# Kernel tuning notes

Measured on AMD Instinct MI355X. Metric: run time of the kernel, lower is better.

Reference implementation:

```python
import jax, jax.numpy as jnp
import numpy as np

N_EMBD = 2048
N_HEAD = 16
N_KV_HEAD = 4
HEAD_DIM = N_EMBD // N_HEAD  # 128
BLOCK_SIZE = 2048
B, T = 4, 2048


def _rope_cache(max_pos, head_dim):
    inv_freq = 1.0 / (10000.0 ** (np.arange(0, head_dim, 2, dtype=np.float32) / head_dim))
    t = np.arange(max_pos, dtype=np.float32)
    freqs = np.repeat(np.outer(t, inv_freq), 2, axis=-1)  # [max_pos, head_dim], interleaved repeat
    return jnp.asarray(np.cos(freqs)), jnp.asarray(np.sin(freqs))

COS, SIN = _rope_cache(BLOCK_SIZE, HEAD_DIM)


def _apply_rope(x, pos):
    # x: [B, nh, T, hd]; matches torch module: cos/sin repeat-interleaved, rotate by halves
    Tq = x.shape[2]
    cos = jax.lax.dynamic_slice_in_dim(COS, pos, Tq, axis=0)[None, None]  # [1,1,T,hd]
    sin = jax.lax.dynamic_slice_in_dim(SIN, pos, Tq, axis=0)[None, None]
    hd = x.shape[-1]
    x1, x2 = x[..., : hd // 2], x[..., hd // 2 :]
    return x * cos + jnp.concatenate([-x2, x1], axis=-1) * sin


def setup_inputs() -> dict:
    key = jax.random.key(0)
    ks = jax.random.split(key, 5)
    scale = 1.0 / np.sqrt(N_EMBD)
    return {
        "x": jax.random.normal(ks[0], (B, T, N_EMBD), dtype=jnp.float32),
        "Wq": jax.random.normal(ks[1], (N_EMBD, N_EMBD), dtype=jnp.float32) * scale,
        "Wk": jax.random.normal(ks[2], (N_EMBD, N_KV_HEAD * HEAD_DIM), dtype=jnp.float32) * scale,
        "Wv": jax.random.normal(ks[3], (N_EMBD, N_KV_HEAD * HEAD_DIM), dtype=jnp.float32) * scale,
        "Wo": jax.random.normal(ks[4], (N_EMBD, N_EMBD), dtype=jnp.float32) * scale,
        "pos": 0,
    }


def reference(x, Wq, Wk, Wv, Wo, pos):
    Bx, Tx, C = x.shape
    q = (x @ Wq).reshape(Bx, Tx, N_HEAD, HEAD_DIM).transpose(0, 2, 1, 3)      # [B,nh,T,hd]
    k = (x @ Wk).reshape(Bx, Tx, N_KV_HEAD, HEAD_DIM).transpose(0, 2, 1, 3)   # [B,nkv,T,hd]
    v = (x @ Wv).reshape(Bx, Tx, N_KV_HEAD, HEAD_DIM).transpose(0, 2, 1, 3)
    q = _apply_rope(q, pos)
    k = _apply_rope(k, pos)
    # GQA: expand kv heads to query heads (cache=None -> causal prefill)
    rep = N_HEAD // N_KV_HEAD
    kr = jnp.repeat(k, rep, axis=1)
    vr = jnp.repeat(v, rep, axis=1)
    scores = jnp.einsum("bhqd,bhkd->bhqk", q, kr) / np.sqrt(HEAD_DIM)
    causal = jnp.tril(jnp.ones((Tx, Tx), dtype=bool))
    scores = jnp.where(causal[None, None], scores, jnp.finfo(scores.dtype).min)
    att = jax.nn.softmax(scores, axis=-1)
    out = jnp.einsum("bhqk,bhkd->bhqd", att, vr)          # [B,nh,T,hd]
    y = out.transpose(0, 2, 1, 3).reshape(Bx, Tx, C)
    return y @ Wo
```

## Files before the change

kernel.cpp:

```cpp
#include <hip/hip_runtime.h>
#include <math.h>

#define TT 2048

typedef __attribute__((ext_vector_type(8))) short bfrag;
typedef __attribute__((ext_vector_type(4))) float facc;

#define NEG_BIG (-1.0e30f)

typedef __attribute__((address_space(1))) const void gas_void;
typedef __attribute__((address_space(3))) void las_void;

__device__ __forceinline__ void gl_lds16(const void* g, void* l) {
    __builtin_amdgcn_global_load_lds((gas_void*)g, (las_void*)l, 16, 0, 0);
}

__device__ __forceinline__ unsigned short f2b(float f) {
    union { float f; unsigned int i; } v; v.f = f;
    unsigned int b = v.i;
    return (unsigned short)((b + 0x7FFFu + ((b >> 16) & 1u)) >> 16);
}
__device__ __forceinline__ void cvt8_f32(const float* __restrict__ p, unsigned short* d) {
    float4 lo = *(const float4*)p, hi = *(const float4*)(p + 4);
    d[0] = f2b(lo.x); d[1] = f2b(lo.y); d[2] = f2b(lo.z); d[3] = f2b(lo.w);
    d[4] = f2b(hi.x); d[5] = f2b(hi.y); d[6] = f2b(hi.z); d[7] = f2b(hi.w);
}

__global__ __launch_bounds__(256) void k_cvt(const float* __restrict__ in,
                                             unsigned short* __restrict__ out, int n8) {
    int c = blockIdx.x * 256 + threadIdx.x;
    if (c < n8) {
        unsigned short t[8];
        cvt8_f32(in + (size_t)c * 8, t);
        *(uint4*)(out + (size_t)c * 8) = *(const uint4*)t;
    }
}

__global__ __launch_bounds__(256) void k_wt(const float* __restrict__ W,
                                            unsigned short* __restrict__ WT, int N) {
    __shared__ alignas(16) unsigned short tile[64][72];
    int r0 = blockIdx.y * 64, c0 = blockIdx.x * 64;
    int tid = threadIdx.x;
    for (int i = 0; i < 2; ++i) {
        int c = tid + i * 256;
        int row = c >> 3, c8 = (c & 7) * 8;
        unsigned short t[8];
        cvt8_f32(W + (size_t)(r0 + row) * N + c0 + c8, t);
        *(uint4*)&tile[row][c8] = *(const uint4*)t;
    }
    __syncthreads();
    for (int i = 0; i < 2; ++i) {
        int c = tid + i * 256;
        int col = c >> 3, r8 = (c & 7) * 8;
        unsigned short t[8];
        for (int j = 0; j < 8; ++j) t[j] = tile[r8 + j][col];
        *(uint4*)(WT + (size_t)(c0 + col) * 2048 + r0 + r8) = *(const uint4*)t;
    }
}

__global__ __launch_bounds__(256) void k_vt(const unsigned short* __restrict__ QKV,
                                            unsigned short* __restrict__ VbT) {
    __shared__ alignas(16) unsigned short tile[64][72];
    int r0 = blockIdx.y * 64, c0 = blockIdx.x * 64;
    int tid = threadIdx.x;
    for (int i = 0; i < 2; ++i) {
        int c = tid + i * 256;
        int row = c >> 3, c8 = (c & 7) * 8;
        *(uint4*)&tile[row][c8] =
            *(const uint4*)(QKV + (size_t)(r0 + row) * 3072 + 2560 + c0 + c8);
    }
    __syncthreads();
    for (int i = 0; i < 2; ++i) {
        int c = tid + i * 256;
        int col = c >> 3, r8 = (c & 7) * 8;
        unsigned short t[8];
        for (int j = 0; j < 8; ++j) t[j] = tile[r8 + j][col];
        *(uint4*)(VbT + (size_t)(c0 + col) * 8192 + r0 + r8) = *(const uint4*)t;
    }
}

__global__ __launch_bounds__(256) void k_gemm2ph(const unsigned short* __restrict__ A,
                                                 const unsigned short* __restrict__ Bt,
                                                 void* __restrict__ Cmat,
                                                 int M, int N, int K, int outF) {
    __shared__ union SM {
        struct { unsigned short A[2][128][64]; unsigned short B[2][128][64]; } s;
        unsigned short ct[32][136];
        float          ctf[32][136];
    } sm;
    int tid = threadIdx.x;
    int w = tid >> 6, lane = tid & 63, quad = lane >> 4, l15 = lane & 15;
    int m0 = blockIdx.y * 128, n0 = blockIdx.x * 128;
    int wm = (w >> 1) * 64, wn = (w & 1) * 64;

    int srow   = lane >> 3;
    int schunk = (lane & 7) ^ (lane >> 3);

    facc acc[4][4];
#pragma unroll
    for (int mi = 0; mi < 4; ++mi)
#pragma unroll
        for (int ni = 0; ni < 4; ++ni)
#pragma unroll
            for (int r = 0; r < 4; ++r) acc[mi][ni][r] = 0.f;

    auto stage = [&](int bb, int k0) {
#pragma unroll
        for (int i = 0; i < 4; ++i) {
            int row = w * 32 + i * 8;
            gl_lds16(A  + (size_t)(m0 + row + srow) * K + k0 + schunk * 8, &sm.s.A[bb][row][0]);
            gl_lds16(Bt + (size_t)(n0 + row + srow) * K + k0 + schunk * 8, &sm.s.B[bb][row][0]);
        }
    };

    int NT = K >> 6;
    stage(0, 0);
    __syncthreads();

    for (int t = 0; t < NT; ++t) {
        int cur = t & 1;
        if (t + 1 < NT) stage(cur ^ 1, (t + 1) * 64);

        bfrag af[4][2], bf[4][2];
#pragma unroll
        for (int mi = 0; mi < 4; ++mi)
#pragma unroll
            for (int kc = 0; kc < 2; ++kc)
                af[mi][kc] = *(const bfrag*)&sm.s.A[cur][wm + mi * 16 + l15][((kc * 4 + quad) ^ (l15 & 7)) * 8];
#pragma unroll
        for (int ni = 0; ni < 4; ++ni)
#pragma unroll
            for (int kc = 0; kc < 2; ++kc)
                bf[ni][kc] = *(const bfrag*)&sm.s.B[cur][wn + ni * 16 + l15][((kc * 4 + quad) ^ (l15 & 7)) * 8];
#pragma unroll
        for (int kc = 0; kc < 2; ++kc)
#pragma unroll
            for (int mi = 0; mi < 4; ++mi)
#pragma unroll
                for (int ni = 0; ni < 4; ++ni)
                    acc[mi][ni] = __builtin_amdgcn_mfma_f32_16x16x32_bf16(af[mi][kc], bf[ni][kc], acc[mi][ni], 0, 0, 0);

        __syncthreads();
    }

#pragma unroll
    for (int t = 0; t < 4; ++t) {
        __syncthreads();
#pragma unroll
        for (int ni = 0; ni < 4; ++ni)
#pragma unroll
            for (int r = 0; r < 4; ++r) {
                int lr = (w >> 1) * 16 + quad * 4 + r;
                int lc = wn + ni * 16 + l15;
                if (outF) sm.ctf[lr][lc] = acc[t][ni][r];
                else      sm.ct [lr][lc] = f2b(acc[t][ni][r]);
            }
        __syncthreads();
        if (outF) {
#pragma unroll
            for (int i = 0; i < 4; ++i) {
                int cc = tid + i * 256;
                int lr = cc >> 5, c4 = (cc & 31) * 4;
                int grow = m0 + (lr >> 4) * 64 + t * 16 + (lr & 15);
                *(float4*)((float*)Cmat + (size_t)grow * N + n0 + c4) =
                    *(const float4*)&sm.ctf[lr][c4];
            }
        } else {
#pragma unroll
            for (int i = 0; i < 2; ++i) {
                int cc = tid + i * 256;
                int lr = cc >> 4, c8 = (cc & 15) * 8;
                int grow = m0 + (lr >> 4) * 64 + t * 16 + (lr & 15);
                *(uint4*)((unsigned short*)Cmat + (size_t)grow * N + n0 + c8) =
                    *(const uint4*)&sm.ct[lr][c8];
            }
        }
    }
}

__global__ __launch_bounds__(256) void k_rope(unsigned short* __restrict__ X,
                                              int lognh, int stride,
                                              const int* __restrict__ posPtr) {
    int tid = blockIdx.x * 256 + threadIdx.x;
    int d = tid & 63;
    int nh = 1 << lognh;
    int h = (tid >> 6) & (nh - 1);
    int row = tid >> (6 + lognh);
    int t = row & (TT - 1);
    float p = (float)(*posPtr + t);
    size_t base = (size_t)row * stride + h * 128 + d;
    union { unsigned int i; float f; } a, b2;
    a.i  = ((unsigned int)X[base]) << 16;
    b2.i = ((unsigned int)X[base + 64]) << 16;
    float x1 = a.f, x2 = b2.f;
    int i1 = d >> 1;
    float f1 = exp2f(-(float)i1 * 0.20762050595278f);
    float f2 = exp2f(-(float)(i1 + 32) * 0.20762050595278f);
    float th1 = p * f1, th2 = p * f2;
    X[base]      = f2b(x1 * cosf(th1) - x2 * sinf(th1));
    X[base + 64] = f2b(x2 * cosf(th2) + x1 * sinf(th2));
}

__device__ __forceinline__ void flash_pass(
    int qbase, int b, int h, int kvh,
    const unsigned short* __restrict__ QKV,
    const unsigned short* __restrict__ VbT,
    unsigned short* __restrict__ att,
    unsigned short (&Ks)[2][32][136],
    unsigned short (&Vt)[2][128][40],
    unsigned short (&Pt)[8][16][40]) {

    int tid = threadIdx.x;
    int w = tid >> 6, lane = tid & 63, quad = lane >> 4, l15 = lane & 15;

    bfrag qf[4];
    {
        size_t qrow = (size_t)(b * TT + qbase + w * 16 + l15);
        for (int kc = 0; kc < 4; ++kc)
            qf[kc] = *(const bfrag*)(QKV + qrow * 3072 + h * 128 + kc * 32 + quad * 8);
    }

    float mreg = NEG_BIG, lreg = 0.f;
    facc o[8];
#pragma unroll
    for (int nb2 = 0; nb2 < 8; ++nb2)
#pragma unroll
        for (int r = 0; r < 4; ++r) o[nb2][r] = 0.f;

    int krow = tid >> 4, d8 = (tid & 15) * 8;
    int vd = tid >> 2, tc = (tid & 3) * 8;
    const unsigned short* Kg = QKV + (size_t)(b * TT) * 3072 + 2048 + kvh * 128;
    const unsigned short* Vg = VbT + (size_t)(kvh * 128 + vd) * 8192 + b * TT;

    const float sc = 0.08838834764831845f;
    int kmax = qbase + 128;
    int nt = kmax >> 5;
    int qgmin = qbase + w * 16;
    int myq = qgmin + l15;

    uint4 rk = *(const uint4*)(Kg + (size_t)krow * 3072 + d8);
    uint4 rv = *(const uint4*)(Vg + tc);

    for (int t = 0; t < nt; ++t) {
        int cur = t & 1;
        int k0 = t * 32;
        *(uint4*)&Ks[cur][krow][d8] = rk;
        *(uint4*)&Vt[cur][vd][tc]   = rv;
        __syncthreads();

        if (t + 1 < nt) {
            int k0n = k0 + 32;
            rk = *(const uint4*)(Kg + (size_t)(k0n + krow) * 3072 + d8);
            rv = *(const uint4*)(Vg + k0n + tc);
        }

        if (k0 > qgmin + 15) continue;

        facc s[2];
#pragma unroll
        for (int nb = 0; nb < 2; ++nb) {
#pragma unroll
            for (int r = 0; r < 4; ++r) s[nb][r] = 0.f;
#pragma unroll
            for (int kc = 0; kc < 4; ++kc) {
                bfrag kf = *(const bfrag*)&Ks[cur][nb * 16 + l15][kc * 32 + quad * 8];
                s[nb] = __builtin_amdgcn_mfma_f32_16x16x32_bf16(kf, qf[kc], s[nb], 0, 0, 0);
            }
        }

        bool fullT = (k0 + 31) <= qgmin;
        float v[2][4];
        if (fullT) {
#pragma unroll
            for (int nb = 0; nb < 2; ++nb)
#pragma unroll
                for (int r = 0; r < 4; ++r) v[nb][r] = s[nb][r] * sc;
        } else {
#pragma unroll
            for (int nb = 0; nb < 2; ++nb)
#pragma unroll
                for (int r = 0; r < 4; ++r) {
                    int kg = k0 + nb * 16 + quad * 4 + r;
                    v[nb][r] = (kg > myq) ? NEG_BIG : s[nb][r] * sc;
                }
        }

        float mx = fmaxf(fmaxf(fmaxf(v[0][0], v[0][1]), fmaxf(v[0][2], v[0][3])),
                         fmaxf(fmaxf(v[1][0], v[1][1]), fmaxf(v[1][2], v[1][3])));
        mx = fmaxf(mx, __shfl_xor(mx, 16, 64));
        mx = fmaxf(mx, __shfl_xor(mx, 32, 64));

        bool need = (mx > mreg + 8.f);
        float mnew = need ? mx : mreg;
        float alpha = need ? __expf(mreg - mnew) : 1.f;

        float p[2][4];
        float psum = 0.f;
#pragma unroll
        for (int nb = 0; nb < 2; ++nb)
#pragma unroll
            for (int r = 0; r < 4; ++r) {
                p[nb][r] = __expf(v[nb][r] - mnew);
                psum += p[nb][r];
            }
        psum += __shfl_xor(psum, 16, 64);
        psum += __shfl_xor(psum, 32, 64);
        lreg = lreg * alpha + psum;
        mreg = mnew;

#pragma unroll
        for (int nb = 0; nb < 2; ++nb) {
            unsigned short pk[4];
#pragma unroll
            for (int r = 0; r < 4; ++r) pk[r] = f2b(p[nb][r]);
            *(uint2*)&Pt[w][l15][nb * 16 + quad * 4] = *(const uint2*)pk;
        }

        if (__any(need)) {
#pragma unroll
            for (int r = 0; r < 4; ++r) {
                float al = __shfl(alpha, quad * 4 + r, 16);
#pragma unroll
                for (int nb2 = 0; nb2 < 8; ++nb2) o[nb2][r] *= al;
            }
        }

        asm volatile("s_waitcnt lgkmcnt(0)" ::: "memory");
        bfrag pf = *(const bfrag*)&Pt[w][l15][quad * 8];
#pragma unroll
        for (int nb2 = 0; nb2 < 8; ++nb2) {
            bfrag vf = *(const bfrag*)&Vt[cur][nb2 * 16 + l15][quad * 8];
            o[nb2] = __builtin_amdgcn_mfma_f32_16x16x32_bf16(pf, vf, o[nb2], 0, 0, 0);
        }
    }

    float lr[4];
#pragma unroll
    for (int r = 0; r < 4; ++r) lr[r] = __shfl(lreg, quad * 4 + r, 16);
#pragma unroll
    for (int nb2 = 0; nb2 < 8; ++nb2)
#pragma unroll
        for (int r = 0; r < 4; ++r) {
            int qg = qbase + w * 16 + quad * 4 + r;
            att[(size_t)(b * TT + qg) * 2048 + h * 128 + nb2 * 16 + l15] =
                f2b(o[nb2][r] / lr[r]);
        }
}

__global__ __launch_bounds__(512, 4) void k_flash(const unsigned short* __restrict__ QKV,
                                                  const unsigned short* __restrict__ VbT,
                                                  unsigned short* __restrict__ att) {
    __shared__ alignas(16) unsigned short Ks[2][32][136];
    __shared__ alignas(16) unsigned short Vt[2][128][40];
    __shared__ alignas(16) unsigned short Pt[8][16][40];
    int bh = blockIdx.y;
    int b = bh >> 4, h = bh & 15;
    int kvh = h >> 2;
    int i = blockIdx.x;

    flash_pass(i * 128, b, h, kvh, QKV, VbT, att, Ks, Vt, Pt);
    __syncthreads();
    flash_pass((15 - i) * 128, b, h, kvh, QKV, VbT, att, Ks, Vt, Pt);
}

extern "C" void kernel_launch(void* const* d_in, const int* in_sizes, int n_in,
                              void* d_out, int out_size, void* d_ws, size_t ws_size,
                              hipStream_t stream) {
    const float* x  = (const float*)d_in[0];
    const float* Wq = (const float*)d_in[1];
    const float* Wk = (const float*)d_in[2];
    const float* Wv = (const float*)d_in[3];
    const float* Wo = (const float*)d_in[4];
    const int* pos  = (const int*)d_in[5];

    char* ws = (char*)d_ws;
    unsigned short* xb   = (unsigned short*)(ws + 0);
    unsigned short* QKV  = (unsigned short*)(ws + 33554432);
    unsigned short* VbT  = (unsigned short*)(ws + 83886080);
    unsigned short* WqT  = (unsigned short*)(ws + 92274688);
    unsigned short* WkvT = (unsigned short*)(ws + 100663296);
    unsigned short* WoT  = (unsigned short*)(ws + 104857600);

    k_cvt<<<8192, 256, 0, stream>>>(x, xb, 2097152);
    k_wt<<<dim3(32, 32), 256, 0, stream>>>(Wq, WqT, 2048);
    k_wt<<<dim3(8, 32),  256, 0, stream>>>(Wk, WkvT, 512);
    k_wt<<<dim3(8, 32),  256, 0, stream>>>(Wv, WkvT + (size_t)512 * 2048, 512);
    k_wt<<<dim3(32, 32), 256, 0, stream>>>(Wo, WoT, 2048);

    k_gemm2ph<<<dim3(24, 64), 256, 0, stream>>>(xb, WqT, QKV, 8192, 3072, 2048, 0);

    k_rope<<<32768, 256, 0, stream>>>(QKV, 4, 3072, pos);
    k_rope<<<8192,  256, 0, stream>>>(QKV + 2048, 2, 3072, pos);

    k_vt<<<dim3(8, 128), 256, 0, stream>>>(QKV, VbT);

    k_flash<<<dim3(8, 64), 512, 0, stream>>>(QKV, VbT, xb);

    k_gemm2ph<<<dim3(16, 64), 256, 0, stream>>>(xb, WoT, d_out, 8192, 2048, 2048, 1);
}
```

Measured before the change: 592.1 us.

## Precompute RoPE trig table, vectorize rope, add MFMA priority and alt LDS swizzle

Measured after the change: 681.1 us. 1.15x slower.

```diff
diff --git a/kernel.cpp b/kernel.cpp
--- a/kernel.cpp
+++ b/kernel.cpp
@@ -19,6 +19,9 @@
     union { float f; unsigned int i; } v; v.f = f;
     unsigned int b = v.i;
     return (unsigned short)((b + 0x7FFFu + ((b >> 16) & 1u)) >> 16);
+}
+__device__ __forceinline__ float b2f(unsigned short s) {
+    union { unsigned int i; float f; } u; u.i = ((unsigned int)s) << 16; return u.f;
 }
 __device__ __forceinline__ void cvt8_f32(const float* __restrict__ p, unsigned short* d) {
     float4 lo = *(const float4*)p, hi = *(const float4*)(p + 4);
@@ -79,6 +82,7 @@
     }
 }
 
+template <int SWZ>
 __global__ __launch_bounds__(256) void k_gemm2ph(const unsigned short* __restrict__ A,
                                                  const unsigned short* __restrict__ Bt,
                                                  void* __restrict__ Cmat,
@@ -94,7 +98,9 @@
     int wm = (w >> 1) * 64, wn = (w & 1) * 64;
 
     int srow   = lane >> 3;
-    int schunk = (lane & 7) ^ (lane >> 3);
+    int schunk = SWZ ? ((lane & 7) ^ ((lane & 32) >> 4))
+                     : ((lane & 7) ^ (lane >> 3));
+    int rsw = SWZ ? ((l15 & 4) >> 1) : (l15 & 7);
 
     facc acc[4][4];
 #pragma unroll
@@ -126,12 +132,12 @@
         for (int mi = 0; mi < 4; ++mi)
 #pragma unroll
             for (int kc = 0; kc < 2; ++kc)
-                af[mi][kc] = *(const bfrag*)&sm.s.A[cur][wm + mi * 16 + l15][((kc * 4 + quad) ^ (l15 & 7)) * 8];
+                af[mi][kc] = *(const bfrag*)&sm.s.A[cur][wm + mi * 16 + l15][(((kc * 4 + quad) ^ rsw)) * 8];
 #pragma unroll
         for (int ni = 0; ni < 4; ++ni)
 #pragma unroll
             for (int kc = 0; kc < 2; ++kc)
-                bf[ni][kc] = *(const bfrag*)&sm.s.B[cur][wn + ni * 16 + l15][((kc * 4 + quad) ^ (l15 & 7)) * 8];
+                bf[ni][kc] = *(const bfrag*)&sm.s.B[cur][wn + ni * 16 + l15][(((kc * 4 + quad) ^ rsw)) * 8];
 #pragma unroll
         for (int kc = 0; kc < 2; ++kc)
 #pragma unroll
@@ -178,27 +184,40 @@
     }
 }
 
-__global__ __launch_bounds__(256) void k_rope(unsigned short* __restrict__ X,
-                                              int lognh, int stride,
+__global__ __launch_bounds__(256) void k_trig(float2* __restrict__ tab,
                                               const int* __restrict__ posPtr) {
     int tid = blockIdx.x * 256 + threadIdx.x;
-    int d = tid & 63;
+    int i1 = tid & 63, t = tid >> 6;
+    float p = (float)(*posPtr + t);
+    float f = exp2f(-(float)i1 * 0.20762050595278f);
+    float th = p * f;
+    tab[tid] = make_float2(cosf(th), sinf(th));
+}
+
+__global__ __launch_bounds__(256) void k_rope(unsigned short* __restrict__ X,
+                                              const float2* __restrict__ tab,
+                                              int lognh, int stride) {
+    int tid = blockIdx.x * 256 + threadIdx.x;
+    int d2 = tid & 31;
     int nh = 1 << lognh;
-    int h = (tid >> 6) & (nh - 1);
-    int row = tid >> (6 + lognh);
+    int h = (tid >> 5) & (nh - 1);
+    int row = tid >> (5 + lognh);
     int t = row & (TT - 1);
-    float p = (float)(*posPtr + t);
-    size_t base = (size_t)row * stride + h * 128 + d;
-    union { unsigned int i; float f; } a, b2;
-    a.i  = ((unsigned int)X[base]) << 16;
-    b2.i = ((unsigned int)X[base + 64]) << 16;
-    float x1 = a.f, x2 = b2.f;
-    int i1 = d >> 1;
-    float f1 = exp2f(-(float)i1 * 0.20762050595278f);
-    float f2 = exp2f(-(float)(i1 + 32) * 0.20762050595278f);
-    float th1 = p * f1, th2 = p * f2;
-    X[base]      = f2b(x1 * cosf(th1) - x2 * sinf(th1));
-    X[base + 64] = f2b(x2 * cosf(th2) + x1 * sinf(th2));
+    size_t base = (size_t)row * stride + h * 128 + d2 * 2;
+    unsigned int ua = *(const unsigned int*)(X + base);
+    unsigned int ub = *(const unsigned int*)(X + base + 64);
+    float x1a = b2f((unsigned short)(ua & 0xffff));
+    float x1b = b2f((unsigned short)(ua >> 16));
+    float x2a = b2f((unsigned short)(ub & 0xffff));
+    float x2b = b2f((unsigned short)(ub >> 16));
+    float2 cs1 = tab[t * 64 + d2];
+    float2 cs2 = tab[t * 64 + d2 + 32];
+    unsigned int o1 = (unsigned int)f2b(x1a * cs1.x - x2a * cs1.y)
+                    | ((unsigned int)f2b(x1b * cs1.x - x2b * cs1.y) << 16);
+    unsigned int o2 = (unsigned int)f2b(x2a * cs2.x + x1a * cs2.y)
+                    | ((unsigned int)f2b(x2b * cs2.x + x1b * cs2.y) << 16);
+    *(unsigned int*)(X + base)      = o1;
+    *(unsigned int*)(X + base + 64) = o2;
 }
 
 __device__ __forceinline__ void flash_pass(
@@ -257,6 +276,7 @@
         if (k0 > qgmin + 15) continue;
 
         facc s[2];
+        __builtin_amdgcn_s_setprio(1);
 #pragma unroll
         for (int nb = 0; nb < 2; ++nb) {
 #pragma unroll
@@ -267,6 +287,7 @@
                 s[nb] = __builtin_amdgcn_mfma_f32_16x16x32_bf16(kf, qf[kc], s[nb], 0, 0, 0);
             }
         }
+        __builtin_amdgcn_s_setprio(0);
 
         bool fullT = (k0 + 31) <= qgmin;
         float v[2][4];
@@ -327,11 +348,13 @@
 
         asm volatile("s_waitcnt lgkmcnt(0)" ::: "memory");
         bfrag pf = *(const bfrag*)&Pt[w][l15][quad * 8];
+        __builtin_amdgcn_s_setprio(1);
 #pragma unroll
         for (int nb2 = 0; nb2 < 8; ++nb2) {
             bfrag vf = *(const bfrag*)&Vt[cur][nb2 * 16 + l15][quad * 8];
             o[nb2] = __builtin_amdgcn_mfma_f32_16x16x32_bf16(pf, vf, o[nb2], 0, 0, 0);
         }
+        __builtin_amdgcn_s_setprio(0);
     }
 
     float lr[4];
@@ -380,6 +403,9 @@
     unsigned short* WqT  = (unsigned short*)(ws + 92274688);
     unsigned short* WkvT = (unsigned short*)(ws + 100663296);
     unsigned short* WoT  = (unsigned short*)(ws + 104857600);
+    float2*         tab  = (float2*)(ws + 113246208);
+
+    k_trig<<<512, 256, 0, stream>>>(tab, pos);
 
     k_cvt<<<8192, 256, 0, stream>>>(x, xb, 2097152);
     k_wt<<<dim3(32, 32), 256, 0, stream>>>(Wq, WqT, 2048);
@@ -387,14 +413,14 @@
     k_wt<<<dim3(8, 32),  256, 0, stream>>>(Wv, WkvT + (size_t)512 * 2048, 512);
     k_wt<<<dim3(32, 32), 256, 0, stream>>>(Wo, WoT, 2048);
 
-    k_gemm2ph<<<dim3(24, 64), 256, 0, stream>>>(xb, WqT, QKV, 8192, 3072, 2048, 0);
-
-    k_rope<<<32768, 256, 0, stream>>>(QKV, 4, 3072, pos);
-    k_rope<<<8192,  256, 0, stream>>>(QKV + 2048, 2, 3072, pos);
+    k_gemm2ph<1><<<dim3(24, 64), 256, 0, stream>>>(xb, WqT, QKV, 8192, 3072, 2048, 0);
+
+    k_rope<<<16384, 256, 0, stream>>>(QKV, tab, 4, 3072);
+    k_rope<<<4096,  256, 0, stream>>>(QKV + 2048, tab, 2, 3072);
 
     k_vt<<<dim3(8, 128), 256, 0, stream>>>(QKV, VbT);
 
     k_flash<<<dim3(8, 64), 512, 0, stream>>>(QKV, VbT, xb);
 
-    k_gemm2ph<<<dim3(16, 64), 256, 0, stream>>>(xb, WoT, d_out, 8192, 2048, 2048, 1);
-}
+    k_gemm2ph<0><<<dim3(16, 64), 256, 0, stream>>>(xb, WoT, d_out, 8192, 2048, 2048, 1);
+}
```
